# Performance work log

Measured on AMD Instinct MI355X. Metric: run time of the kernel, lower is better.

The kernel has to match this reference:

```python
import jax, jax.numpy as jnp
import numpy as np

A, B = 0.0, 1.0
U_LEFT, U_RIGHT = 0.0, 0.0
BOUNDARY_PENALTY = 10.0
N_POINTS = 32768
K_TEST = 1024  # sine test functions
LAYERS = [1, 256, 256, 256, 1]


def setup_inputs() -> dict:
    key = jax.random.key(0)
    ks = jax.random.split(key, 2 + len(LAYERS) - 1)
    # Gauss-Lobatto-like nodes: sorted points in (A, B)
    x = jnp.sort(jax.random.uniform(ks[0], (N_POINTS, 1), dtype=jnp.float32,
                                    minval=A, maxval=B), axis=0)
    # positive quadrature weights, scaled so sum(weights) ~ (B - A)
    weights = jax.random.uniform(ks[1], (N_POINTS,), dtype=jnp.float32) * (2.0 * (B - A) / N_POINTS)
    inp = {"x": x, "weights": weights}
    for i in range(len(LAYERS) - 1):
        fin, fout = LAYERS[i], LAYERS[i + 1]
        inp[f"W{i}"] = jax.random.normal(ks[2 + i], (fin, fout), dtype=jnp.float32) / np.sqrt(fin).astype(np.float32)
        inp[f"b{i}"] = jnp.zeros((fout,), dtype=jnp.float32)
    return inp


def _mlp(h, params):
    # tanh MLP, no activation on the last layer (matches MLP.forward)
    n = len(params)
    for i, (W, b) in enumerate(params):
        h = h @ W + b
        if i < n - 1:
            h = jnp.tanh(h)
    return h


def reference(x, weights, W0, b0, W1, b1, W2, b2, W3, b3):
    params = [(W0, b0), (W1, b1), (W2, b2), (W3, b3)]
    xf = x[:, 0]                                   # [N]

    u = _mlp(x, params)                            # [N, 1]

    # u_xx at every quadrature node via grad-of-grad, vmapped over points
    def u_scalar(xv):
        return _mlp(xv.reshape(1, 1), params)[0, 0]
    u_xx = jax.vmap(jax.grad(jax.grad(u_scalar)))(xf)   # [N]

    # analytic sine test functions v_k(x) = sin(pi k x), k = 1..K
    k = jnp.arange(1, K_TEST + 1, dtype=x.dtype)        # [K]
    test = jnp.sin(jnp.pi * k[:, None] * xf[None, :])   # [K, N]

    source = jnp.sin(jnp.pi * xf)                       # f(x) on the grid, [N]

    # batched quadrature: one matvec replaces the per-k Integrate loop
    Fk = test @ (weights * source)                      # [K]
    Rk = -(test @ (weights * u_xx))                     # [K]  (method 1: -int u_xx v_k)

    loss_interior = jnp.mean((Rk - Fk) ** 2)
    loss_boundary = 0.5 * BOUNDARY_PENALTY * (
        (u[0, 0] - U_LEFT) ** 2 + (u[-1, 0] - U_RIGHT) ** 2
    )
    return jnp.stack([loss_interior, loss_boundary])
```

## Files before the change

kernel.cpp:

```cpp
#include <hip/hip_runtime.h>
#include <cmath>

#define N_PTS 32768
#define HID   256
#define KTEST 1024
#define MB    32
#define RS    264
#define SKC   256
#define SKYB  (N_PTS / SKC)
#define SKGRID (4 * SKYB)

typedef float  f32x4  __attribute__((ext_vector_type(4)));
typedef short  s16x8  __attribute__((ext_vector_type(8)));
typedef __bf16 bf16x8 __attribute__((ext_vector_type(8)));

__device__ __forceinline__ float b2f(unsigned short s) {
    return __uint_as_float(((unsigned int)s) << 16);
}
__device__ __forceinline__ unsigned short cvt16(float x) {
    return __builtin_bit_cast(unsigned short, (__bf16)x);
}
__device__ __forceinline__ void split2(float x, unsigned short& hi, unsigned short& lo) {
    unsigned int b = __float_as_uint(x);
    hi = (unsigned short)(b >> 16);
    float hf = __uint_as_float(b & 0xFFFF0000u);
    lo = cvt16(x - hf);
}
__device__ __forceinline__ float fast_tanh(float z) {
    float e = __expf(2.0f * z);
    return 1.0f - 2.0f / (e + 1.0f);
}

__global__ __launch_bounds__(64) void wswz_kernel(
    const float* __restrict__ W1, const float* __restrict__ W2,
    unsigned short* __restrict__ Wh1, unsigned short* __restrict__ Wl1,
    unsigned short* __restrict__ Wh2, unsigned short* __restrict__ Wl2,
    unsigned int* __restrict__ counter)
{
    const int lane = threadIdx.x;
    const int t  = blockIdx.x;
    const int kc = blockIdx.y;
    const float* W = blockIdx.z ? W2 : W1;
    unsigned short* Wh = blockIdx.z ? Wh2 : Wh1;
    unsigned short* Wl = blockIdx.z ? Wl2 : Wl1;
    const int q = lane >> 4, ln = lane & 15;
    const int n = t * 16 + ln;
    const int kbase = kc * 32 + q * 8;

    s16x8 hv, lv;
    #pragma unroll
    for (int j = 0; j < 8; ++j) {
        unsigned short h, l;
        split2(W[(kbase + j) * HID + n], h, l);
        hv[j] = (short)h; lv[j] = (short)l;
    }
    const int out = ((t * 8 + kc) * 64 + lane) * 8;
    *(s16x8*)(Wh + out) = hv;
    *(s16x8*)(Wl + out) = lv;

    if (lane == 0 && t == 0 && kc == 0 && blockIdx.z == 0)
        *counter = 0u;
}

__global__ __launch_bounds__(512, 4) void mlp_kernel(
    const float* __restrict__ x, const float* __restrict__ wq,
    const float* __restrict__ W0, const float* __restrict__ b0,
    const float* __restrict__ b1v, const float* __restrict__ b2v,
    const float* __restrict__ W3, const float* __restrict__ b3,
    const unsigned short* __restrict__ W1h, const unsigned short* __restrict__ W1l,
    const unsigned short* __restrict__ W2h, const unsigned short* __restrict__ W2l,
    float* __restrict__ u_arr, float* __restrict__ d_arr)
{
    __shared__ __align__(16) unsigned short Hb[3][MB][RS];

    const int tid = threadIdx.x;
    const int gp0 = blockIdx.x * MB;

    {
        const int m = tid & 31, jseg = tid >> 5;
        const float xm = x[gp0 + m];
        #pragma unroll 4
        for (int jj = 0; jj < 16; ++jj) {
            int j = jseg * 16 + jj;
            float w = W0[j];
            float z = fmaf(xm, w, b0[j]);
            float y = fast_tanh(z);
            float s = 1.0f - y * y;
            float yp = s * w;
            float ypp = -2.0f * y * yp * w;
            Hb[0][m][j] = cvt16(y);
            Hb[1][m][j] = cvt16(yp);
            Hb[2][m][j] = cvt16(ypp);
        }
    }
    __syncthreads();

    const int lane = tid & 63, wv = tid >> 6;
    const int q = lane >> 4, ln = lane & 15;

    const int fragbase = (wv * 2) * 8 * 512 + lane * 8;

    for (int layer = 0; layer < 2; ++layer) {
        const unsigned short* __restrict__ WhW = (layer ? W2h : W1h) + fragbase;
        const unsigned short* __restrict__ WlW = (layer ? W2l : W1l) + fragbase;
        const float* __restrict__ bb = layer ? b2v : b1v;

        f32x4 acc[3][2][2];
        #pragma unroll
        for (int s = 0; s < 3; ++s)
            #pragma unroll
            for (int mf = 0; mf < 2; ++mf)
                #pragma unroll
                for (int nt = 0; nt < 2; ++nt)
                    acc[s][mf][nt] = (f32x4){0.f, 0.f, 0.f, 0.f};

        s16x8 bh[2][2], bl[2][2];
        #pragma unroll
        for (int nt = 0; nt < 2; ++nt) {
            bh[0][nt] = *(const s16x8*)(WhW + nt * 4096);
            bl[0][nt] = *(const s16x8*)(WlW + nt * 4096);
        }

        int cur = 0;
        for (int kc = 0; kc < 8; ++kc) {
            const int nxt = cur ^ 1;
            if (kc < 7) {
                #pragma unroll
                for (int nt = 0; nt < 2; ++nt) {
                    const int off = nt * 4096 + (kc + 1) * 512;
                    bh[nxt][nt] = *(const s16x8*)(WhW + off);
                    bl[nxt][nt] = *(const s16x8*)(WlW + off);
                }
            }
            s16x8 av[3][2];
            #pragma unroll
            for (int s = 0; s < 3; ++s)
                #pragma unroll
                for (int mf = 0; mf < 2; ++mf)
                    av[s][mf] = *(const s16x8*)&Hb[s][mf * 16 + ln][kc * 32 + q * 8];
            #pragma unroll
            for (int s = 0; s < 3; ++s)
                #pragma unroll
                for (int mf = 0; mf < 2; ++mf)
                    #pragma unroll
                    for (int nt = 0; nt < 2; ++nt) {
                        acc[s][mf][nt] = __builtin_amdgcn_mfma_f32_16x16x32_bf16(
                            __builtin_bit_cast(bf16x8, av[s][mf]),
                            __builtin_bit_cast(bf16x8, bh[cur][nt]), acc[s][mf][nt], 0, 0, 0);
                        acc[s][mf][nt] = __builtin_amdgcn_mfma_f32_16x16x32_bf16(
                            __builtin_bit_cast(bf16x8, av[s][mf]),
                            __builtin_bit_cast(bf16x8, bl[cur][nt]), acc[s][mf][nt], 0, 0, 0);
                    }
            cur = nxt;
        }
        __syncthreads();

        #pragma unroll
        for (int nt = 0; nt < 2; ++nt) {
            const int c = wv * 32 + nt * 16 + ln;
            const float bias = bb[c];
            #pragma unroll
            for (int mf = 0; mf < 2; ++mf) {
                #pragma unroll
                for (int i = 0; i < 4; ++i) {
                    const int r = mf * 16 + q * 4 + i;
                    float z   = acc[0][mf][nt][i] + bias;
                    float zp  = acc[1][mf][nt][i];
                    float zpp = acc[2][mf][nt][i];
                    float y  = fast_tanh(z);
                    float s  = 1.0f - y * y;
                    float yp = s * zp;
                    float ypp = fmaf(s, zpp, -2.0f * y * yp * zp);
                    Hb[0][r][c] = cvt16(y);
                    if (layer == 0) Hb[1][r][c] = cvt16(yp);
                    Hb[2][r][c] = cvt16(ypp);
                }
            }
        }
        __syncthreads();
    }

    float* psum = (float*)&Hb[1][0][0];
    {
        const int m = tid & 31, seg = tid >> 5;
        float su = 0.f, sx = 0.f;
        #pragma unroll 4
        for (int jj = 0; jj < 16; ++jj) {
            int j = seg * 16 + jj;
            float w3 = W3[j];
            su = fmaf(b2f(Hb[0][m][j]), w3, su);
            sx = fmaf(b2f(Hb[2][m][j]), w3, sx);
        }
        psum[(0 * 16 + seg) * 32 + m] = su;
        psum[(1 * 16 + seg) * 32 + m] = sx;
    }
    __syncthreads();
    if (tid < MB) {
        float u = b3[0], uxx = 0.f;
        #pragma unroll
        for (int s2 = 0; s2 < 16; ++s2) {
            u   += psum[s2 * 32 + tid];
            uxx += psum[(16 + s2) * 32 + tid];
        }
        const int gp = gp0 + tid;
        u_arr[gp] = u;
        float xv = x[gp];
        d_arr[gp] = -wq[gp] * (uxx + sinpif(xv));
    }
}

__global__ __launch_bounds__(256) void sk_loss_kernel(
    const float* __restrict__ x, const float* __restrict__ d_arr,
    const float* __restrict__ u_arr, float* __restrict__ part,
    unsigned int* __restrict__ counter, float* __restrict__ out)
{
    __shared__ float xs_h[SKC], xs_l[SKC], ds[SKC];
    __shared__ float red[4];
    __shared__ int lastFlag;

    const int tid = threadIdx.x;
    const int k = blockIdx.x * 256 + tid;
    const int i0 = blockIdx.y * SKC;

    {
        float xv = x[i0 + tid];
        float xh = __uint_as_float(__float_as_uint(xv) & 0xFFFFF000u);
        xs_h[tid] = xh * 0.5f;
        xs_l[tid] = (xv - xh) * 0.5f;
        ds[tid]   = d_arr[i0 + tid];
    }
    __syncthreads();

    const float kf = (float)(k + 1);
    float s = 0.f;
    #pragma unroll 8
    for (int i = 0; i < SKC; ++i) {
        float A = kf * xs_h[i];
        float f = __builtin_amdgcn_fractf(A);
        float t = __builtin_amdgcn_fractf(fmaf(kf, xs_l[i], f));
        s = fmaf(__builtin_amdgcn_sinf(t), ds[i], s);
    }
    part[blockIdx.y * KTEST + k] = s;

    __threadfence();
    if (tid == 0)
        lastFlag = (atomicAdd(counter, 1u) == (unsigned)(SKGRID - 1));
    __syncthreads();
    if (!lastFlag) return;
    __threadfence();

    float a0 = 0.f, a1 = 0.f, a2 = 0.f, a3 = 0.f;
    const float* P = part + tid * 4;
    for (int yb = 0; yb < SKYB; ++yb) {
        f32x4 v = *(const f32x4*)(P + yb * KTEST);
        a0 += v[0]; a1 += v[1]; a2 += v[2]; a3 += v[3];
    }
    float sq = a0 * a0 + a1 * a1 + a2 * a2 + a3 * a3;
    #pragma unroll
    for (int off = 32; off > 0; off >>= 1) sq += __shfl_down(sq, off, 64);
    if ((tid & 63) == 0) red[tid >> 6] = sq;
    __syncthreads();
    if (tid == 0) {
        float t = red[0] + red[1] + red[2] + red[3];
        out[0] = t * (1.0f / (float)KTEST);
        float u0 = u_arr[0], uN = u_arr[N_PTS - 1];
        out[1] = 5.0f * (u0 * u0 + uN * uN);
    }
}

extern "C" void kernel_launch(void* const* d_in, const int* in_sizes, int n_in,
                              void* d_out, int out_size, void* d_ws, size_t ws_size,
                              hipStream_t stream)
{
    const float* x  = (const float*)d_in[0];
    const float* wq = (const float*)d_in[1];
    const float* W0 = (const float*)d_in[2];
    const float* b0 = (const float*)d_in[3];
    const float* W1 = (const float*)d_in[4];
    const float* b1 = (const float*)d_in[5];
    const float* W2 = (const float*)d_in[6];
    const float* b2 = (const float*)d_in[7];
    const float* W3 = (const float*)d_in[8];
    const float* b3 = (const float*)d_in[9];
    float* out = (float*)d_out;

    float* ws    = (float*)d_ws;
    float* u_arr = ws;
    float* d_arr = ws + N_PTS;
    float* part  = ws + 2 * N_PTS;
    unsigned short* W1h = (unsigned short*)(ws + 2 * N_PTS + SKYB * KTEST);
    unsigned short* W1l = W1h + HID * HID;
    unsigned short* W2h = W1l + HID * HID;
    unsigned short* W2l = W2h + HID * HID;
    unsigned int* counter = (unsigned int*)(W2l + HID * HID);

    wswz_kernel<<<dim3(16, 8, 2), 64, 0, stream>>>(W1, W2, W1h, W1l, W2h, W2l, counter);
    mlp_kernel<<<N_PTS / MB, 512, 0, stream>>>(x, wq, W0, b0, b1, b2, W3, b3,
                                               W1h, W1l, W2h, W2l, u_arr, d_arr);
    sk_loss_kernel<<<dim3(4, SKYB), 256, 0, stream>>>(x, d_arr, u_arr, part, counter, out);
}
```

Baseline: 163.9 us.

## Switch MLP matmuls to 32x32x16 MFMA and vectorize LDS accesses

Replaces the 16x16x32 bf16 MFMA tiling in the hidden layers with 32x32x16 MFMAs, so each wave covers its 32x32 output tile with one accumulator per stream. The weight swizzle kernel is rewritten to match the new B-fragment layout. Layer-0 writes, the final W3 reduction and the sine-sum kernel's shared loads are also vectorized to cut LDS instruction count. The larger MFMA shape means fewer instructions and A-fragment reloads, but the epilogue's LDS writes follow a different row pattern that could hit more bank conflicts.

```diff
diff --git a/kernel.cpp b/kernel.cpp
--- a/kernel.cpp
+++ b/kernel.cpp
@@ -11,6 +11,8 @@
 #define SKGRID (4 * SKYB)
 
 typedef float  f32x4  __attribute__((ext_vector_type(4)));
+typedef float  f32x16 __attribute__((ext_vector_type(16)));
+typedef short  s16x4  __attribute__((ext_vector_type(4)));
 typedef short  s16x8  __attribute__((ext_vector_type(8)));
 typedef __bf16 bf16x8 __attribute__((ext_vector_type(8)));
 
@@ -43,20 +45,23 @@
     const float* W = blockIdx.z ? W2 : W1;
     unsigned short* Wh = blockIdx.z ? Wh2 : Wh1;
     unsigned short* Wl = blockIdx.z ? Wl2 : Wl1;
-    const int q = lane >> 4, ln = lane & 15;
-    const int n = t * 16 + ln;
-    const int kbase = kc * 32 + q * 8;
-
-    s16x8 hv, lv;
+    const int h = lane >> 5, c = lane & 31;
+    const int col = t * 32 + c;
+
     #pragma unroll
-    for (int j = 0; j < 8; ++j) {
-        unsigned short h, l;
-        split2(W[(kbase + j) * HID + n], h, l);
-        hv[j] = (short)h; lv[j] = (short)l;
-    }
-    const int out = ((t * 8 + kc) * 64 + lane) * 8;
-    *(s16x8*)(Wh + out) = hv;
-    *(s16x8*)(Wl + out) = lv;
+    for (int ks = 0; ks < 2; ++ks) {
+        const int kb = kc * 32 + ks * 16 + h * 8;
+        s16x8 hv, lv;
+        #pragma unroll
+        for (int j = 0; j < 8; ++j) {
+            unsigned short hh, ll;
+            split2(W[(kb + j) * HID + col], hh, ll);
+            hv[j] = (short)hh; lv[j] = (short)ll;
+        }
+        const int out = (((t * 8 + kc) * 2 + ks) * 64 + lane) * 8;
+        *(s16x8*)(Wh + out) = hv;
+        *(s16x8*)(Wl + out) = lv;
+    }
 
     if (lane == 0 && t == 0 && kc == 0 && blockIdx.z == 0)
         *counter = 0u;
@@ -77,48 +82,49 @@
     const int gp0 = blockIdx.x * MB;
 
     {
-        const int m = tid & 31, jseg = tid >> 5;
+        const int m = tid & 31, seg = tid >> 5;
         const float xm = x[gp0 + m];
-        #pragma unroll 4
-        for (int jj = 0; jj < 16; ++jj) {
-            int j = jseg * 16 + jj;
-            float w = W0[j];
-            float z = fmaf(xm, w, b0[j]);
-            float y = fast_tanh(z);
-            float s = 1.0f - y * y;
-            float yp = s * w;
-            float ypp = -2.0f * y * yp * w;
-            Hb[0][m][j] = cvt16(y);
-            Hb[1][m][j] = cvt16(yp);
-            Hb[2][m][j] = cvt16(ypp);
+        #pragma unroll
+        for (int jb = 0; jb < 4; ++jb) {
+            s16x4 vy, vyp, vypp;
+            #pragma unroll
+            for (int jl = 0; jl < 4; ++jl) {
+                const int j = seg * 16 + jb * 4 + jl;
+                float w = W0[j];
+                float z = fmaf(xm, w, b0[j]);
+                float y = fast_tanh(z);
+                float s = 1.0f - y * y;
+                float yp = s * w;
+                float ypp = -2.0f * y * yp * w;
+                vy[jl]   = (short)cvt16(y);
+                vyp[jl]  = (short)cvt16(yp);
+                vypp[jl] = (short)cvt16(ypp);
+            }
+            const int j0 = seg * 16 + jb * 4;
+            *(s16x4*)&Hb[0][m][j0] = vy;
+            *(s16x4*)&Hb[1][m][j0] = vyp;
+            *(s16x4*)&Hb[2][m][j0] = vypp;
         }
     }
     __syncthreads();
 
     const int lane = tid & 63, wv = tid >> 6;
-    const int q = lane >> 4, ln = lane & 15;
-
-    const int fragbase = (wv * 2) * 8 * 512 + lane * 8;
+    const int c32 = lane & 31, h = lane >> 5;
+
+    const int fragbase = wv * 8192 + lane * 8;
 
     for (int layer = 0; layer < 2; ++layer) {
         const unsigned short* __restrict__ WhW = (layer ? W2h : W1h) + fragbase;
         const unsigned short* __restrict__ WlW = (layer ? W2l : W1l) + fragbase;
         const float* __restrict__ bb = layer ? b2v : b1v;
 
-        f32x4 acc[3][2][2];
-        #pragma unroll
-        for (int s = 0; s < 3; ++s)
-            #pragma unroll
-            for (int mf = 0; mf < 2; ++mf)
-                #pragma unroll
-                for (int nt = 0; nt < 2; ++nt)
-                    acc[s][mf][nt] = (f32x4){0.f, 0.f, 0.f, 0.f};
+        f32x16 acc[3] = {};
 
         s16x8 bh[2][2], bl[2][2];
         #pragma unroll
-        for (int nt = 0; nt < 2; ++nt) {
-            bh[0][nt] = *(const s16x8*)(WhW + nt * 4096);
-            bl[0][nt] = *(const s16x8*)(WlW + nt * 4096);
+        for (int ks = 0; ks < 2; ++ks) {
+            bh[0][ks] = *(const s16x8*)(WhW + ks * 512);
+            bl[0][ks] = *(const s16x8*)(WlW + ks * 512);
         }
 
         int cur = 0;
@@ -126,55 +132,53 @@
             const int nxt = cur ^ 1;
             if (kc < 7) {
                 #pragma unroll
-                for (int nt = 0; nt < 2; ++nt) {
-                    const int off = nt * 4096 + (kc + 1) * 512;
-                    bh[nxt][nt] = *(const s16x8*)(WhW + off);
-                    bl[nxt][nt] = *(const s16x8*)(WlW + off);
+                for (int ks = 0; ks < 2; ++ks) {
+                    const int off = (kc + 1) * 1024 + ks * 512;
+                    bh[nxt][ks] = *(const s16x8*)(WhW + off);
+                    bl[nxt][ks] = *(const s16x8*)(WlW + off);
                 }
             }
             s16x8 av[3][2];
             #pragma unroll
             for (int s = 0; s < 3; ++s)
                 #pragma unroll
-                for (int mf = 0; mf < 2; ++mf)
-                    av[s][mf] = *(const s16x8*)&Hb[s][mf * 16 + ln][kc * 32 + q * 8];
-            #pragma unroll
-            for (int s = 0; s < 3; ++s)
-                #pragma unroll
-                for (int mf = 0; mf < 2; ++mf)
-                    #pragma unroll
-                    for (int nt = 0; nt < 2; ++nt) {
-                        acc[s][mf][nt] = __builtin_amdgcn_mfma_f32_16x16x32_bf16(
-                            __builtin_bit_cast(bf16x8, av[s][mf]),
-                            __builtin_bit_cast(bf16x8, bh[cur][nt]), acc[s][mf][nt], 0, 0, 0);
-                        acc[s][mf][nt] = __builtin_amdgcn_mfma_f32_16x16x32_bf16(
-                            __builtin_bit_cast(bf16x8, av[s][mf]),
-                            __builtin_bit_cast(bf16x8, bl[cur][nt]), acc[s][mf][nt], 0, 0, 0);
-                    }
+                for (int ks = 0; ks < 2; ++ks)
+                    av[s][ks] = *(const s16x8*)&Hb[s][c32][kc * 32 + ks * 16 + h * 8];
+            #pragma unroll
+            for (int s = 0; s < 3; ++s) {
+                acc[s] = __builtin_amdgcn_mfma_f32_32x32x16_bf16(
+                    __builtin_bit_cast(bf16x8, av[s][0]),
+                    __builtin_bit_cast(bf16x8, bh[cur][0]), acc[s], 0, 0, 0);
+                acc[s] = __builtin_amdgcn_mfma_f32_32x32x16_bf16(
+                    __builtin_bit_cast(bf16x8, av[s][1]),
+                    __builtin_bit_cast(bf16x8, bh[cur][1]), acc[s], 0, 0, 0);
+                acc[s] = __builtin_amdgcn_mfma_f32_32x32x16_bf16(
+                    __builtin_bit_cast(bf16x8, av[s][0]),
+                    __builtin_bit_cast(bf16x8, bl[cur][0]), acc[s], 0, 0, 0);
+                acc[s] = __builtin_amdgcn_mfma_f32_32x32x16_bf16(
+                    __builtin_bit_cast(bf16x8, av[s][1]),
+                    __builtin_bit_cast(bf16x8, bl[cur][1]), acc[s], 0, 0, 0);
+            }
             cur = nxt;
         }
         __syncthreads();
 
-        #pragma unroll
-        for (int nt = 0; nt < 2; ++nt) {
-            const int c = wv * 32 + nt * 16 + ln;
+        {
+            const int c = wv * 32 + c32;
             const float bias = bb[c];
             #pragma unroll
-            for (int mf = 0; mf < 2; ++mf) {
-                #pragma unroll
-                for (int i = 0; i < 4; ++i) {
-                    const int r = mf * 16 + q * 4 + i;
-                    float z   = acc[0][mf][nt][i] + bias;
-                    float zp  = acc[1][mf][nt][i];
-                    float zpp = acc[2][mf][nt][i];
-                    float y  = fast_tanh(z);
-                    float s  = 1.0f - y * y;
-                    float yp = s * zp;
-                    float ypp = fmaf(s, zpp, -2.0f * y * yp * zp);
-                    Hb[0][r][c] = cvt16(y);
-                    if (layer == 0) Hb[1][r][c] = cvt16(yp);
-                    Hb[2][r][c] = cvt16(ypp);
-                }
+            for (int reg = 0; reg < 16; ++reg) {
+                const int r = (reg & 3) + 8 * (reg >> 2) + 4 * h;
+                float z   = acc[0][reg] + bias;
+                float zp  = acc[1][reg];
+                float zpp = acc[2][reg];
+                float y  = fast_tanh(z);
+                float s  = 1.0f - y * y;
+                float yp = s * zp;
+                float ypp = fmaf(s, zpp, -2.0f * y * yp * zp);
+                Hb[0][r][c] = cvt16(y);
+                if (layer == 0) Hb[1][r][c] = cvt16(yp);
+                Hb[2][r][c] = cvt16(ypp);
             }
         }
         __syncthreads();
@@ -184,12 +188,17 @@
     {
         const int m = tid & 31, seg = tid >> 5;
         float su = 0.f, sx = 0.f;
-        #pragma unroll 4
-        for (int jj = 0; jj < 16; ++jj) {
-            int j = seg * 16 + jj;
-            float w3 = W3[j];
-            su = fmaf(b2f(Hb[0][m][j]), w3, su);
-            sx = fmaf(b2f(Hb[2][m][j]), w3, sx);
+        #pragma unroll
+        for (int jj8 = 0; jj8 < 2; ++jj8) {
+            const int j0 = seg * 16 + jj8 * 8;
+            s16x8 vy = *(const s16x8*)&Hb[0][m][j0];
+            s16x8 vx = *(const s16x8*)&Hb[2][m][j0];
+            #pragma unroll
+            for (int u = 0; u < 8; ++u) {
+                float w3 = W3[j0 + u];
+                su = fmaf(b2f((unsigned short)vy[u]), w3, su);
+                sx = fmaf(b2f((unsigned short)vx[u]), w3, sx);
+            }
         }
         psum[(0 * 16 + seg) * 32 + m] = su;
         psum[(1 * 16 + seg) * 32 + m] = sx;
@@ -214,7 +223,7 @@
     const float* __restrict__ u_arr, float* __restrict__ part,
     unsigned int* __restrict__ counter, float* __restrict__ out)
 {
-    __shared__ float xs_h[SKC], xs_l[SKC], ds[SKC];
+    __shared__ __align__(16) float xs4[SKC][4];
     __shared__ float red[4];
     __shared__ int lastFlag;
 
@@ -225,9 +234,12 @@
     {
         float xv = x[i0 + tid];
         float xh = __uint_as_float(__float_as_uint(xv) & 0xFFFFF000u);
-        xs_h[tid] = xh * 0.5f;
-        xs_l[tid] = (xv - xh) * 0.5f;
-        ds[tid]   = d_arr[i0 + tid];
+        f32x4 w;
+        w[0] = xh * 0.5f;
+        w[1] = (xv - xh) * 0.5f;
+        w[2] = d_arr[i0 + tid];
+        w[3] = 0.f;
+        *(f32x4*)xs4[tid] = w;
     }
     __syncthreads();
 
@@ -235,10 +247,11 @@
     float s = 0.f;
     #pragma unroll 8
     for (int i = 0; i < SKC; ++i) {
-        float A = kf * xs_h[i];
+        const f32x4 v = *(const f32x4*)xs4[i];
+        float A = kf * v[0];
         float f = __builtin_amdgcn_fractf(A);
-        float t = __builtin_amdgcn_fractf(fmaf(kf, xs_l[i], f));
-        s = fmaf(__builtin_amdgcn_sinf(t), ds[i], s);
+        float t = __builtin_amdgcn_fractf(fmaf(kf, v[1], f));
+        s = fmaf(__builtin_amdgcn_sinf(t), v[2], s);
     }
     part[blockIdx.y * KTEST + k] = s;
 
@@ -294,7 +307,7 @@
     unsigned short* W2l = W2h + HID * HID;
     unsigned int* counter = (unsigned int*)(W2l + HID * HID);
 
-    wswz_kernel<<<dim3(16, 8, 2), 64, 0, stream>>>(W1, W2, W1h, W1l, W2h, W2l, counter);
+    wswz_kernel<<<dim3(8, 8, 2), 64, 0, stream>>>(W1, W2, W1h, W1l, W2h, W2l, counter);
     mlp_kernel<<<N_PTS / MB, 512, 0, stream>>>(x, wq, W0, b0, b1, b2, W3, b3,
                                                W1h, W1l, W2h, W2l, u_arr, d_arr);
     sk_loss_kernel<<<dim3(4, SKYB), 256, 0, stream>>>(x, d_arr, u_arr, part, counter, out);
```

Result: slower. 170.9 us (+4.2%).

## Fuse sine-test quadrature into MLP kernel with per-block partials and reduction

Applied to the files above, without the earlier changes.

Moves the sine-test-function projection into the tail of the MLP kernel. Each 32-point block computes partial sums for all 1024 test functions using hardware fract/sin on split-precision x, then writes them to a per-block partial buffer that a new reduction kernel sums and squares. This removes the separate sk_loss pass over d_arr and x. The cost is a 4 MB partial buffer that is written and read back, plus extra work and one more barrier inside the MLP kernel. The change also vectorizes the layer-0 LDS stores and the final W3 dot-product LDS loads.

```diff
diff --git a/kernel.cpp b/kernel.cpp
--- a/kernel.cpp
+++ b/kernel.cpp
@@ -9,8 +9,10 @@
 #define SKC   256
 #define SKYB  (N_PTS / SKC)
 #define SKGRID (4 * SKYB)
+#define NBLK  (N_PTS / MB)
 
 typedef float  f32x4  __attribute__((ext_vector_type(4)));
+typedef short  s16x4  __attribute__((ext_vector_type(4)));
 typedef short  s16x8  __attribute__((ext_vector_type(8)));
 typedef __bf16 bf16x8 __attribute__((ext_vector_type(8)));
 
@@ -69,28 +71,38 @@
     const float* __restrict__ W3, const float* __restrict__ b3,
     const unsigned short* __restrict__ W1h, const unsigned short* __restrict__ W1l,
     const unsigned short* __restrict__ W2h, const unsigned short* __restrict__ W2l,
-    float* __restrict__ u_arr, float* __restrict__ d_arr)
+    float* __restrict__ u_arr, float* __restrict__ d_arr,
+    float* __restrict__ partF)
 {
     __shared__ __align__(16) unsigned short Hb[3][MB][RS];
+    __shared__ float sx_h[MB], sx_l[MB], sd[MB];
 
     const int tid = threadIdx.x;
     const int gp0 = blockIdx.x * MB;
 
     {
-        const int m = tid & 31, jseg = tid >> 5;
+        const int m = tid & 31, seg = tid >> 5;
         const float xm = x[gp0 + m];
-        #pragma unroll 4
-        for (int jj = 0; jj < 16; ++jj) {
-            int j = jseg * 16 + jj;
-            float w = W0[j];
-            float z = fmaf(xm, w, b0[j]);
-            float y = fast_tanh(z);
-            float s = 1.0f - y * y;
-            float yp = s * w;
-            float ypp = -2.0f * y * yp * w;
-            Hb[0][m][j] = cvt16(y);
-            Hb[1][m][j] = cvt16(yp);
-            Hb[2][m][j] = cvt16(ypp);
+        #pragma unroll
+        for (int jb = 0; jb < 4; ++jb) {
+            s16x4 vy, vyp, vypp;
+            #pragma unroll
+            for (int jl = 0; jl < 4; ++jl) {
+                const int j = seg * 16 + jb * 4 + jl;
+                float w = W0[j];
+                float z = fmaf(xm, w, b0[j]);
+                float y = fast_tanh(z);
+                float s = 1.0f - y * y;
+                float yp = s * w;
+                float ypp = -2.0f * y * yp * w;
+                vy[jl]   = (short)cvt16(y);
+                vyp[jl]  = (short)cvt16(yp);
+                vypp[jl] = (short)cvt16(ypp);
+            }
+            const int j0 = seg * 16 + jb * 4;
+            *(s16x4*)&Hb[0][m][j0] = vy;
+            *(s16x4*)&Hb[1][m][j0] = vyp;
+            *(s16x4*)&Hb[2][m][j0] = vypp;
         }
     }
     __syncthreads();
@@ -184,12 +196,17 @@
     {
         const int m = tid & 31, seg = tid >> 5;
         float su = 0.f, sx = 0.f;
-        #pragma unroll 4
-        for (int jj = 0; jj < 16; ++jj) {
-            int j = seg * 16 + jj;
-            float w3 = W3[j];
-            su = fmaf(b2f(Hb[0][m][j]), w3, su);
-            sx = fmaf(b2f(Hb[2][m][j]), w3, sx);
+        #pragma unroll
+        for (int jj8 = 0; jj8 < 2; ++jj8) {
+            const int j0 = seg * 16 + jj8 * 8;
+            s16x8 vy = *(const s16x8*)&Hb[0][m][j0];
+            s16x8 vx = *(const s16x8*)&Hb[2][m][j0];
+            #pragma unroll
+            for (int u = 0; u < 8; ++u) {
+                float w3 = W3[j0 + u];
+                su = fmaf(b2f((unsigned short)vy[u]), w3, su);
+                sx = fmaf(b2f((unsigned short)vx[u]), w3, sx);
+            }
         }
         psum[(0 * 16 + seg) * 32 + m] = su;
         psum[(1 * 16 + seg) * 32 + m] = sx;
@@ -205,7 +222,79 @@
         const int gp = gp0 + tid;
         u_arr[gp] = u;
         float xv = x[gp];
-        d_arr[gp] = -wq[gp] * (uxx + sinpif(xv));
+        float dv = -wq[gp] * (uxx + sinpif(xv));
+        d_arr[gp] = dv;
+        float xh = __uint_as_float(__float_as_uint(xv) & 0xFFFFF000u);
+        sx_h[tid] = xh * 0.5f;
+        sx_l[tid] = (xv - xh) * 0.5f;
+        sd[tid]   = dv;
+    }
+
+    if (partF) {
+        __syncthreads();
+        const float k1 = (float)(tid + 1);
+        const float k2 = (float)(tid + 513);
+        float s1 = 0.f, s2 = 0.f;
+        #pragma unroll 8
+        for (int i = 0; i < MB; ++i) {
+            float xh = sx_h[i], xl = sx_l[i], dv = sd[i];
+            float f1 = __builtin_amdgcn_fractf(k1 * xh);
+            float t1 = __builtin_amdgcn_fractf(fmaf(k1, xl, f1));
+            s1 = fmaf(__builtin_amdgcn_sinf(t1), dv, s1);
+            float f2 = __builtin_amdgcn_fractf(k2 * xh);
+            float t2 = __builtin_amdgcn_fractf(fmaf(k2, xl, f2));
+            s2 = fmaf(__builtin_amdgcn_sinf(t2), dv, s2);
+        }
+        partF[blockIdx.x * KTEST + tid]       = s1;
+        partF[blockIdx.x * KTEST + tid + 512] = s2;
+    }
+}
+
+__global__ __launch_bounds__(256) void reduce_kernel(
+    const float* __restrict__ part, const float* __restrict__ u_arr,
+    unsigned int* __restrict__ counter, float* __restrict__ red_g,
+    float* __restrict__ out)
+{
+    __shared__ float sm[8][33];
+    __shared__ int lastFlag;
+
+    const int tid = threadIdx.x;
+    const int kk = tid & 31;
+    const int ch = tid >> 5;
+    const int k = blockIdx.x * 32 + kk;
+
+    const float* P = part + (ch << 7) * KTEST + k;
+    float s = 0.f;
+    #pragma unroll 8
+    for (int b = 0; b < 128; ++b) s += P[b << 10];
+    sm[ch][kk] = s;
+    __syncthreads();
+
+    if (tid < 32) {
+        float t = 0.f;
+        #pragma unroll
+        for (int j = 0; j < 8; ++j) t += sm[j][kk];
+        float sq = t * t;
+        #pragma unroll
+        for (int off = 16; off > 0; off >>= 1) sq += __shfl_down(sq, off, 64);
+        if (kk == 0) red_g[blockIdx.x] = sq;
+    }
+    __threadfence();
+    if (tid == 0)
+        lastFlag = (atomicAdd(counter, 1u) == 31u);
+    __syncthreads();
+    if (!lastFlag) return;
+    __threadfence();
+
+    if (tid < 32) {
+        float v = red_g[tid];
+        #pragma unroll
+        for (int off = 16; off > 0; off >>= 1) v += __shfl_down(v, off, 64);
+        if (tid == 0) {
+            out[0] = v * (1.0f / (float)KTEST);
+            float u0 = u_arr[0], uN = u_arr[N_PTS - 1];
+            out[1] = 5.0f * (u0 * u0 + uN * uN);
+        }
     }
 }
 
@@ -287,15 +376,23 @@
     float* ws    = (float*)d_ws;
     float* u_arr = ws;
     float* d_arr = ws + N_PTS;
-    float* part  = ws + 2 * N_PTS;
+    float* partS = ws + 2 * N_PTS;
     unsigned short* W1h = (unsigned short*)(ws + 2 * N_PTS + SKYB * KTEST);
     unsigned short* W1l = W1h + HID * HID;
     unsigned short* W2h = W1l + HID * HID;
     unsigned short* W2l = W2h + HID * HID;
     unsigned int* counter = (unsigned int*)(W2l + HID * HID);
+    float* red_g = ws + 327696;
+    float* partF = ws + 327744;
+    const size_t need = (size_t)(327744 + NBLK * KTEST) * sizeof(float);
+    const bool fused = ws_size >= need;
 
     wswz_kernel<<<dim3(16, 8, 2), 64, 0, stream>>>(W1, W2, W1h, W1l, W2h, W2l, counter);
-    mlp_kernel<<<N_PTS / MB, 512, 0, stream>>>(x, wq, W0, b0, b1, b2, W3, b3,
-                                               W1h, W1l, W2h, W2l, u_arr, d_arr);
-    sk_loss_kernel<<<dim3(4, SKYB), 256, 0, stream>>>(x, d_arr, u_arr, part, counter, out);
-}
+    mlp_kernel<<<NBLK, 512, 0, stream>>>(x, wq, W0, b0, b1, b2, W3, b3,
+                                         W1h, W1l, W2h, W2l, u_arr, d_arr,
+                                         fused ? partF : nullptr);
+    if (fused)
+        reduce_kernel<<<32, 256, 0, stream>>>(partF, u_arr, counter, red_g, out);
+    else
+        sk_loss_kernel<<<dim3(4, SKYB), 256, 0, stream>>>(x, d_arr, u_arr, partS, counter, out);
+}
```

New measurement: 131.4 us. -19.8%, faster.
